# Kernel tuning notes

Hardware: AMD Instinct MI355X
Metric: run time of the kernel (lower is better)

Reference implementation:

```python
import jax, jax.numpy as jnp
import numpy as np

NUM_HEADS = 16
HEAD_DIM = 64  # hidden_size // num_heads


def _logsparse_allowed(seq_len):
    # allowed[i, j] True if key j is attended by query i:
    # j == i, j == i-1, or j == i - 2^k (k >= 1); combined with causal (j <= i).
    i = jnp.arange(seq_len)[:, None]
    j = jnp.arange(seq_len)[None, :]
    diff = i - j
    pow2 = (diff > 0) & ((diff & (diff - 1)) == 0)  # covers diff==1 and diff==2^k
    return (diff == 0) | pow2  # implies diff >= 0, so causal is subsumed


def setup_inputs() -> dict:
    key = jax.random.key(0)
    ks = jax.random.split(key, 7)
    B, S, H = 4, 2048, 1024
    return {
        "hidden_states": jax.random.normal(ks[0], (B, S, H), dtype=jnp.float32),
        "attention_mask": jnp.zeros((B, 1, 1, S), dtype=jnp.float32),
        "Wq": jax.random.normal(ks[1], (H, H), dtype=jnp.float32) * 0.02,
        "bq": jnp.zeros((H,), dtype=jnp.float32),
        "Wk": jax.random.normal(ks[2], (H, H), dtype=jnp.float32) * 0.02,
        "bk": jnp.zeros((H,), dtype=jnp.float32),
        "Wv": jax.random.normal(ks[3], (H, H), dtype=jnp.float32) * 0.02,
        "bv": jnp.zeros((H,), dtype=jnp.float32),
    }


def _split_heads(x):
    B, S, _ = x.shape
    return x.reshape(B, S, NUM_HEADS, HEAD_DIM).transpose(0, 2, 1, 3)  # b h t d


def reference(hidden_states, attention_mask, Wq, bq, Wk, bk, Wv, bv):
    B, S, H = hidden_states.shape
    q = _split_heads(hidden_states @ Wq.T + bq)
    k = _split_heads(hidden_states @ Wk.T + bk)
    v = _split_heads(hidden_states @ Wv.T + bv)

    scores = jnp.einsum("bhqd,bhkd->bhqk", q, k) * (HEAD_DIM ** -0.5)
    allowed = _logsparse_allowed(S)  # [S, S] bool
    scores = jnp.where(allowed[None, None], scores, -jnp.inf)
    scores = scores + attention_mask  # [B,1,1,S] additive mask
    probs = jax.nn.softmax(scores, axis=-1)
    out = jnp.einsum("bhqk,bhkd->bhqd", probs, v)
    return out.transpose(0, 2, 1, 3).reshape(B, S, H)
```

## Files before the change

kernel.cpp:

```cpp
#include <hip/hip_runtime.h>
#include <hip/hip_bf16.h>

#define S_LEN   2048
#define NHEADS  16
#define HDIM    64
#define HID     1024
#define BATCH   4
#define M_ROWS  (BATCH * S_LEN)

#define BM 128
#define BN 128
#define BK 64

typedef __attribute__((ext_vector_type(8))) short short8;
typedef __attribute__((ext_vector_type(4))) float floatx4;
typedef __attribute__((ext_vector_type(16))) float floatx16;
typedef __attribute__((ext_vector_type(4))) unsigned short ushort4v;

__device__ __forceinline__ unsigned short f2bf_rne(float x) {
  union { float f; unsigned u; } v; v.f = x;
  unsigned r = v.u + 0x7fffu + ((v.u >> 16) & 1u);
  return (unsigned short)(r >> 16);
}

__device__ __forceinline__ float bf2f(unsigned short u) {
  union { unsigned u; float f; } c; c.u = ((unsigned)u) << 16;
  return c.f;
}

__device__ __forceinline__ void glds16(const unsigned short* g, unsigned short* l) {
  __builtin_amdgcn_global_load_lds(
      (const __attribute__((address_space(1))) unsigned int*)g,
      (__attribute__((address_space(3))) unsigned int*)l, 16, 0, 0);
}

#define HS4 (M_ROWS * HID / 4)
#define W4  (HID * HID / 4)
__global__ __launch_bounds__(256) void cast_all(
    const float* __restrict__ hs, const float* __restrict__ Wq,
    const float* __restrict__ Wk, const float* __restrict__ Wv,
    unsigned short* __restrict__ hsb, unsigned short* __restrict__ wqb,
    unsigned short* __restrict__ wkb, unsigned short* __restrict__ wvb) {
  int idx = blockIdx.x * 256 + threadIdx.x;
  const float* in;
  unsigned short* out;
  int off;
  if (idx < HS4) {
    in = hs; out = hsb; off = idx;
  } else {
    int r = idx - HS4;
    int seg = r >> 18;
    off = r & (W4 - 1);
    in  = (seg == 0) ? Wq  : (seg == 1) ? Wk  : Wv;
    out = (seg == 0) ? wqb : (seg == 1) ? wkb : wvb;
  }
  floatx4 v = __builtin_nontemporal_load((const floatx4*)in + off);
  ushort4v o;
  o.x = f2bf_rne(v.x);
  o.y = f2bf_rne(v.y);
  o.z = f2bf_rne(v.z);
  o.w = f2bf_rne(v.w);
  ((ushort4v*)out)[off] = o;
}

__global__ __launch_bounds__(256) void qkv_gemm(
    const unsigned short* __restrict__ A,
    const unsigned short* __restrict__ W0, const unsigned short* __restrict__ W1,
    const unsigned short* __restrict__ W2,
    const float* __restrict__ b0, const float* __restrict__ b1,
    const float* __restrict__ b2,
    unsigned short* __restrict__ O0, unsigned short* __restrict__ O1,
    unsigned short* __restrict__ O2) {
  const int K = HID;
  const int N = HID;
  const int z = blockIdx.z;
  const unsigned short* __restrict__ W = (z == 0) ? W0 : (z == 1) ? W1 : W2;
  const float* __restrict__ bias = (z == 0) ? b0 : (z == 1) ? b1 : b2;
  unsigned short* __restrict__ O = (z == 0) ? O0 : (z == 1) ? O1 : O2;

  __shared__ __align__(16) unsigned short As[BM * BK];
  __shared__ __align__(16) unsigned short Bs[BN * BK];

  const int tid = threadIdx.x;
  const int w = tid >> 6;
  const int lane = tid & 63;
  const int m0 = blockIdx.x * BM;
  const int n0 = blockIdx.y * BN;

  const int lr = lane >> 3;
  const unsigned short* gA[4];
  const unsigned short* gB[4];
  unsigned short* lA[4];
  unsigned short* lB[4];
  #pragma unroll
  for (int u = 0; u < 4; ++u) {
    const int seg = w * 4 + u;
    const int cc = (lane & 7) ^ lr ^ (2 * (seg & 3));
    const int r = seg * 8 + lr;
    gA[u] = A + (size_t)(m0 + r) * K + cc * 8;
    gB[u] = W + (size_t)(n0 + r) * K + cc * 8;
    lA[u] = As + seg * 512;
    lB[u] = Bs + seg * 512;
  }

  const int lrow32 = lane & 31;
  const int kgrp = lane >> 5;
  const int sw = (lane & 7) ^ (2 * ((lane >> 3) & 3));
  const int arow = (w & 1) * 64;
  const int brow = (w >> 1) * 64;

  floatx16 acc[2][2] = {};

  for (int k0 = 0; k0 < K; k0 += BK) {
    #pragma unroll
    for (int u = 0; u < 4; ++u) {
      glds16(gA[u] + k0, lA[u]);
      glds16(gB[u] + k0, lB[u]);
    }
    __syncthreads();

    #pragma unroll
    for (int s = 0; s < 4; ++s) {
      const int cp = (((s << 1) | kgrp) ^ sw) * 8;
      short8 af[2], bf[2];
      #pragma unroll
      for (int im = 0; im < 2; ++im)
        af[im] = *(const short8*)(As + (arow + im * 32 + lrow32) * BK + cp);
      #pragma unroll
      for (int in = 0; in < 2; ++in)
        bf[in] = *(const short8*)(Bs + (brow + in * 32 + lrow32) * BK + cp);

      #pragma unroll
      for (int im = 0; im < 2; ++im)
        #pragma unroll
        for (int in = 0; in < 2; ++in)
          acc[im][in] = __builtin_amdgcn_mfma_f32_32x32x16_bf16(af[im], bf[in], acc[im][in], 0, 0, 0);
    }
    __syncthreads();
  }

  #pragma unroll
  for (int im = 0; im < 2; ++im) {
    #pragma unroll
    for (int in = 0; in < 2; ++in) {
      const int col = n0 + brow + in * 32 + lrow32;
      const float bb = bias[col];
      const int rowbase = m0 + arow + im * 32 + 4 * kgrp;
      #pragma unroll
      for (int reg = 0; reg < 16; ++reg) {
        const int row = rowbase + (reg & 3) + 8 * (reg >> 2);
        O[(size_t)row * N + col] = f2bf_rne(acc[im][in][reg] + bb);
      }
    }
  }
}

__global__ __launch_bounds__(256) void logsparse_attn(
    const unsigned short* __restrict__ Q, const unsigned short* __restrict__ K,
    const unsigned short* __restrict__ V, const float* __restrict__ mask,
    float* __restrict__ out) {
  const int bid = (blockIdx.x & 7) * 512 + (blockIdx.x >> 3);
  const int tid = threadIdx.x;
  const int l = tid & 7;
  const int g = tid >> 3;
  const int h = g & 15;
  const int pair = bid * 2 + (g >> 4);
  const int i = pair & (S_LEN - 1);
  const int b = pair >> 11;

  const size_t rowb = (size_t)b * S_LEN * HID;
  const int co = h * HDIM + l * 8;

  int js[12];
  js[0] = i;
  int nj = 1;
  for (int d = 1; d <= i; d <<= 1) js[nj++] = i - d;
  #pragma unroll
  for (int t = 0; t < 12; ++t)
    if (t >= nj) js[t] = i;

  short8 k8[12];
  #pragma unroll
  for (int t = 0; t < 12; ++t)
    k8[t] = *(const short8*)(K + rowb + (size_t)js[t] * HID + co);
  const short8 q8 = *(const short8*)(Q + rowb + (size_t)i * HID + co);
  float mk[12];
  #pragma unroll
  for (int t = 0; t < 12; ++t)
    mk[t] = mask[b * S_LEN + js[t]];

  float qf[8];
  #pragma unroll
  for (int e = 0; e < 8; ++e) qf[e] = bf2f((unsigned short)q8[e]);

  float s[12];
  #pragma unroll
  for (int t = 0; t < 12; ++t) {
    float p = 0.f;
    #pragma unroll
    for (int e = 0; e < 8; ++e) p += qf[e] * bf2f((unsigned short)k8[t][e]);
    p += __shfl_xor(p, 1, 64);
    p += __shfl_xor(p, 2, 64);
    p += __shfl_xor(p, 4, 64);
    s[t] = (t < nj) ? (p * 0.125f + mk[t]) : -1e30f;
  }

  float mx = s[0];
  #pragma unroll
  for (int t = 1; t < 12; ++t) mx = fmaxf(mx, s[t]);
  float lsum = 0.f;
  #pragma unroll
  for (int t = 0; t < 12; ++t) { s[t] = __expf(s[t] - mx); lsum += s[t]; }
  const float inv = 1.f / lsum;

  short8 v8[12];
  #pragma unroll
  for (int t = 0; t < 12; ++t)
    v8[t] = *(const short8*)(V + rowb + (size_t)js[t] * HID + co);

  float o[8] = {};
  #pragma unroll
  for (int t = 0; t < 12; ++t) {
    #pragma unroll
    for (int e = 0; e < 8; ++e) o[e] += s[t] * bf2f((unsigned short)v8[t][e]);
  }

  float* op = out + rowb + (size_t)i * HID + co;
  floatx4 o0 = {o[0] * inv, o[1] * inv, o[2] * inv, o[3] * inv};
  floatx4 o1 = {o[4] * inv, o[5] * inv, o[6] * inv, o[7] * inv};
  __builtin_nontemporal_store(o0, (floatx4*)op);
  __builtin_nontemporal_store(o1, (floatx4*)(op + 4));
}

extern "C" void kernel_launch(void* const* d_in, const int* in_sizes, int n_in,
                              void* d_out, int out_size, void* d_ws, size_t ws_size,
                              hipStream_t stream) {
  const float* hs   = (const float*)d_in[0];
  const float* mask = (const float*)d_in[1];
  const float* Wq   = (const float*)d_in[2];
  const float* bq   = (const float*)d_in[3];
  const float* Wk   = (const float*)d_in[4];
  const float* bk   = (const float*)d_in[5];
  const float* Wv   = (const float*)d_in[6];
  const float* bv   = (const float*)d_in[7];
  float* out = (float*)d_out;

  unsigned short* hsb = (unsigned short*)d_ws;
  unsigned short* wqb = hsb + (size_t)M_ROWS * HID;
  unsigned short* wkb = wqb + (size_t)HID * HID;
  unsigned short* wvb = wkb + (size_t)HID * HID;
  unsigned short* Qb = wvb + (size_t)HID * HID;
  unsigned short* Kb = Qb + (size_t)M_ROWS * HID;
  unsigned short* Vb = Kb + (size_t)M_ROWS * HID;

  {
    int quads = HS4 + 3 * W4;
    cast_all<<<quads / 256, 256, 0, stream>>>(hs, Wq, Wk, Wv, hsb, wqb, wkb, wvb);
  }

  {
    dim3 grid(M_ROWS / BM, HID / BN, 3);
    qkv_gemm<<<grid, 256, 0, stream>>>(hsb, wqb, wkb, wvb, bq, bk, bv, Qb, Kb, Vb);
  }

  {
    int blocks = (BATCH * S_LEN) / 2;
    logsparse_attn<<<blocks, 256, 0, stream>>>(Qb, Kb, Vb, mask, out);
  }
}
```

Measured before the change: 183.4 us.

## Tile logsparse attention per head and stage nearby K/V rows in LDS

The attention kernel now assigns each block a tile of 128 queries for a single batch and head. It stages the 256 K and V rows covering offsets up to 128 back into shared memory via direct global-to-LDS loads. The first nine log-sparse neighbours, which are within 128 positions, are read from LDS, and the farther ones still come from global memory. This cuts redundant global and L2 traffic for K/V rows shared across nearby queries, at the cost of fewer, larger blocks, 64 KB of LDS per block limiting occupancy, and an upfront load plus barrier.

```diff
diff --git a/kernel.cpp b/kernel.cpp
--- a/kernel.cpp
+++ b/kernel.cpp
@@ -11,6 +11,8 @@
 #define BM 128
 #define BN 128
 #define BK 64
+
+#define TI 128
 
 typedef __attribute__((ext_vector_type(8))) short short8;
 typedef __attribute__((ext_vector_type(4))) float floatx4;
@@ -159,77 +161,111 @@
     const unsigned short* __restrict__ Q, const unsigned short* __restrict__ K,
     const unsigned short* __restrict__ V, const float* __restrict__ mask,
     float* __restrict__ out) {
-  const int bid = (blockIdx.x & 7) * 512 + (blockIdx.x >> 3);
+  __shared__ __align__(16) unsigned short Ks[256 * 64];
+  __shared__ __align__(16) unsigned short Vs[256 * 64];
+
+  const int x = blockIdx.x;
+  const int tile = x & 15;
+  const int h = (x >> 4) & 15;
+  const int b = x >> 8;
+  const int base = tile * TI;
   const int tid = threadIdx.x;
+
+  const size_t bhead = (size_t)b * S_LEN * HID + h * HDIM;
+
+  {
+    const int wv = tid >> 6, ln = tid & 63;
+    const int frow = ln >> 3;
+    const int fcol = (ln & 7) * 8;
+    #pragma unroll
+    for (int u = 0; u < 8; ++u) {
+      const int seg = wv * 8 + u;
+      int gs = base - 128 + seg * 8 + frow;
+      gs = gs < 0 ? 0 : gs;
+      const size_t goff = bhead + (size_t)gs * HID + fcol;
+      glds16(K + goff, Ks + seg * 512);
+      glds16(V + goff, Vs + seg * 512);
+    }
+  }
+  __syncthreads();
+
+  const int g = tid >> 3;
   const int l = tid & 7;
-  const int g = tid >> 3;
-  const int h = g & 15;
-  const int pair = bid * 2 + (g >> 4);
-  const int i = pair & (S_LEN - 1);
-  const int b = pair >> 11;
-
-  const size_t rowb = (size_t)b * S_LEN * HID;
   const int co = h * HDIM + l * 8;
 
-  int js[12];
-  js[0] = i;
-  int nj = 1;
-  for (int d = 1; d <= i; d <<= 1) js[nj++] = i - d;
-  #pragma unroll
-  for (int t = 0; t < 12; ++t)
-    if (t >= nj) js[t] = i;
-
-  short8 k8[12];
-  #pragma unroll
-  for (int t = 0; t < 12; ++t)
-    k8[t] = *(const short8*)(K + rowb + (size_t)js[t] * HID + co);
-  const short8 q8 = *(const short8*)(Q + rowb + (size_t)i * HID + co);
-  float mk[12];
-  #pragma unroll
-  for (int t = 0; t < 12; ++t)
-    mk[t] = mask[b * S_LEN + js[t]];
-
-  float qf[8];
-  #pragma unroll
-  for (int e = 0; e < 8; ++e) qf[e] = bf2f((unsigned short)q8[e]);
-
-  float s[12];
-  #pragma unroll
-  for (int t = 0; t < 12; ++t) {
-    float p = 0.f;
-    #pragma unroll
-    for (int e = 0; e < 8; ++e) p += qf[e] * bf2f((unsigned short)k8[t][e]);
-    p += __shfl_xor(p, 1, 64);
-    p += __shfl_xor(p, 2, 64);
-    p += __shfl_xor(p, 4, 64);
-    s[t] = (t < nj) ? (p * 0.125f + mk[t]) : -1e30f;
-  }
-
-  float mx = s[0];
-  #pragma unroll
-  for (int t = 1; t < 12; ++t) mx = fmaxf(mx, s[t]);
-  float lsum = 0.f;
-  #pragma unroll
-  for (int t = 0; t < 12; ++t) { s[t] = __expf(s[t] - mx); lsum += s[t]; }
-  const float inv = 1.f / lsum;
-
-  short8 v8[12];
-  #pragma unroll
-  for (int t = 0; t < 12; ++t)
-    v8[t] = *(const short8*)(V + rowb + (size_t)js[t] * HID + co);
-
-  float o[8] = {};
-  #pragma unroll
-  for (int t = 0; t < 12; ++t) {
-    #pragma unroll
-    for (int e = 0; e < 8; ++e) o[e] += s[t] * bf2f((unsigned short)v8[t][e]);
-  }
-
-  float* op = out + rowb + (size_t)i * HID + co;
-  floatx4 o0 = {o[0] * inv, o[1] * inv, o[2] * inv, o[3] * inv};
-  floatx4 o1 = {o[4] * inv, o[5] * inv, o[6] * inv, o[7] * inv};
-  __builtin_nontemporal_store(o0, (floatx4*)op);
-  __builtin_nontemporal_store(o1, (floatx4*)(op + 4));
+  for (int c = 0; c < 4; ++c) {
+    const int i = base + c * 32 + g;
+
+    int js[12];
+    js[0] = i;
+    int nj = 1;
+    for (int d = 1; d <= i; d <<= 1) js[nj++] = i - d;
+    #pragma unroll
+    for (int t = 0; t < 12; ++t)
+      if (t >= nj) js[t] = i;
+
+    short8 k8[12];
+    #pragma unroll
+    for (int t = 0; t < 9; ++t) {
+      const int lrow = js[t] - base + 128;
+      k8[t] = *(const short8*)(Ks + lrow * 64 + l * 8);
+    }
+    #pragma unroll
+    for (int t = 9; t < 12; ++t)
+      k8[t] = *(const short8*)(K + bhead + (size_t)js[t] * HID + l * 8);
+    const short8 q8 = *(const short8*)(Q + bhead + (size_t)i * HID + l * 8);
+    float mk[12];
+    #pragma unroll
+    for (int t = 0; t < 12; ++t)
+      mk[t] = mask[b * S_LEN + js[t]];
+
+    float qf[8];
+    #pragma unroll
+    for (int e = 0; e < 8; ++e) qf[e] = bf2f((unsigned short)q8[e]);
+
+    float s[12];
+    #pragma unroll
+    for (int t = 0; t < 12; ++t) {
+      float p = 0.f;
+      #pragma unroll
+      for (int e = 0; e < 8; ++e) p += qf[e] * bf2f((unsigned short)k8[t][e]);
+      p += __shfl_xor(p, 1, 64);
+      p += __shfl_xor(p, 2, 64);
+      p += __shfl_xor(p, 4, 64);
+      s[t] = (t < nj) ? (p * 0.125f + mk[t]) : -1e30f;
+    }
+
+    float mx = s[0];
+    #pragma unroll
+    for (int t = 1; t < 12; ++t) mx = fmaxf(mx, s[t]);
+    float lsum = 0.f;
+    #pragma unroll
+    for (int t = 0; t < 12; ++t) { s[t] = __expf(s[t] - mx); lsum += s[t]; }
+    const float inv = 1.f / lsum;
+
+    short8 v8[12];
+    #pragma unroll
+    for (int t = 0; t < 9; ++t) {
+      const int lrow = js[t] - base + 128;
+      v8[t] = *(const short8*)(Vs + lrow * 64 + l * 8);
+    }
+    #pragma unroll
+    for (int t = 9; t < 12; ++t)
+      v8[t] = *(const short8*)(V + bhead + (size_t)js[t] * HID + l * 8);
+
+    float o[8] = {};
+    #pragma unroll
+    for (int t = 0; t < 12; ++t) {
+      #pragma unroll
+      for (int e = 0; e < 8; ++e) o[e] += s[t] * bf2f((unsigned short)v8[t][e]);
+    }
+
+    float* op = out + bhead + (size_t)i * HID + l * 8;
+    floatx4 o0 = {o[0] * inv, o[1] * inv, o[2] * inv, o[3] * inv};
+    floatx4 o1 = {o[4] * inv, o[5] * inv, o[6] * inv, o[7] * inv};
+    __builtin_nontemporal_store(o0, (floatx4*)op);
+    __builtin_nontemporal_store(o1, (floatx4*)(op + 4));
+  }
 }
 
 extern "C" void kernel_launch(void* const* d_in, const int* in_sizes, int n_in,
@@ -264,7 +300,7 @@
   }
 
   {
-    int blocks = (BATCH * S_LEN) / 2;
+    int blocks = BATCH * NHEADS * (S_LEN / TI);
     logsparse_attn<<<blocks, 256, 0, stream>>>(Qb, Kb, Vb, mask, out);
   }
 }
```

New measurement: 193.2 us. 1.05x slower.
